# Kernel tuning notes

Measured on AMD Instinct MI355X. Metric: run time of the kernel, lower is better.

## Reference

```python
import jax, jax.numpy as jnp
import numpy as np

TOP_K = 2


def setup_inputs() -> dict:
    key = jax.random.key(0)
    ks = jax.random.split(key, 7)
    B, S, D, E = 8, 2048, 1024, 8
    scale = 1.0 / np.sqrt(D)
    return {
        "X": jax.random.normal(ks[0], (B, S, D), dtype=jnp.float32),
        "We": jax.random.normal(ks[1], (E, D, D), dtype=jnp.float32) * scale,
        "be": jax.random.normal(ks[2], (E, D), dtype=jnp.float32) * scale,
        "Wr": jax.random.normal(ks[3], (E, D), dtype=jnp.float32) * scale,
        "br": jax.random.normal(ks[4], (E,), dtype=jnp.float32) * scale,
        "Wo": jax.random.normal(ks[5], (D, D), dtype=jnp.float32) * scale,
        "bo": jax.random.normal(ks[6], (D,), dtype=jnp.float32) * scale,
    }


def reference(X, We, be, Wr, br, Wo, bo):
    # Router: logits [B, S, E] -> softmax -> top-k
    router_logits = jnp.einsum("bsd,ed->bse", X, Wr) + br
    router_weights = jax.nn.softmax(router_logits, axis=-1)
    top_k_weights, top_k_indices = jax.lax.top_k(router_weights, TOP_K)  # [B,S,K]

    # Every expert Linear applied to all tokens (matches original's dense-per-expert math).
    # expert_outputs: [B, S, E, D]
    expert_outputs = jnp.einsum("bsd,ehd->bseh", X, We) + be

    # Gather the top-k experts per token and combine with router weights.
    # gathered: [B, S, K, D]
    gathered = jnp.take_along_axis(expert_outputs, top_k_indices[..., None], axis=2)
    combined = jnp.sum(top_k_weights[..., None] * gathered, axis=2)  # [B, S, D]

    # Output projection
    out = jnp.einsum("bsd,hd->bsh", combined, Wo) + bo
    return out
```

## Files before the change

kernel.cpp:

```cpp
#include <hip/hip_runtime.h>
#include <stdint.h>

#define T_TOK 16384
#define D_DIM 1024
#define E_NUM 8
#define NTILE 264

typedef __attribute__((ext_vector_type(4))) float f32x4;
typedef __attribute__((ext_vector_type(8))) __bf16 bf16x8;
typedef __attribute__((ext_vector_type(4))) unsigned short u16x4;
typedef const __attribute__((address_space(1))) void* gas_ptr;
typedef __attribute__((address_space(3))) void* las_ptr;

#define WS_Y     0ULL
#define WS_ATOK  67108864ULL
#define WS_AW    (WS_ATOK + 131072ULL)
#define WS_SCHED (WS_AW + 131072ULL)
#define WS_TMP   (WS_SCHED + 8192ULL)
#define WS_TKI   WS_TMP
#define WS_TKW   (WS_TKI + 131072ULL)
#define WS_CNTS  (WS_TKW + 131072ULL)
#define WS_BASE  (WS_CNTS + 8192ULL)
#define WS_WOB   WS_TMP


__device__ __forceinline__ unsigned short f2b(float f){
  unsigned int u = __float_as_uint(f);
  u = (u + 0x7FFFu + ((u >> 16) & 1u)) >> 16;
  return (unsigned short)u;
}

__global__ __launch_bounds__(256) void k_router(const float* __restrict__ X,
    const float* __restrict__ Wr, const float* __restrict__ br,
    unsigned short* __restrict__ Xb, int* __restrict__ tki, float* __restrict__ tkw)
{
  const int wv = threadIdx.x >> 6, lane = threadIdx.x & 63;
  const int t = blockIdx.x * 4 + wv;
  const float* x = X + (size_t)t * D_DIM;
  unsigned short* xb = Xb + (size_t)t * D_DIM;
  float acc[E_NUM] = {};
  #pragma unroll
  for (int c = 0; c < 4; ++c){
    const int d = c * 256 + lane * 4;
    f32x4 xv = *reinterpret_cast<const f32x4*>(x + d);
    u16x4 o;
    o[0]=f2b(xv[0]); o[1]=f2b(xv[1]); o[2]=f2b(xv[2]); o[3]=f2b(xv[3]);
    *reinterpret_cast<u16x4*>(xb + d) = o;
    #pragma unroll
    for (int e = 0; e < E_NUM; ++e){
      f32x4 w4 = *reinterpret_cast<const f32x4*>(Wr + e * D_DIM + d);
      acc[e] += xv[0]*w4[0] + xv[1]*w4[1] + xv[2]*w4[2] + xv[3]*w4[3];
    }
  }
  #pragma unroll
  for (int e = 0; e < E_NUM; ++e){
    float v = acc[e];
    #pragma unroll
    for (int off = 32; off >= 1; off >>= 1) v += __shfl_xor(v, off, 64);
    acc[e] = v + br[e];
  }
  int i1 = 0; float l1 = acc[0];
  #pragma unroll
  for (int e = 1; e < E_NUM; ++e) if (acc[e] > l1){ l1 = acc[e]; i1 = e; }
  int i2 = -1; float l2 = -3.4e38f;
  #pragma unroll
  for (int e = 0; e < E_NUM; ++e) if (e != i1 && acc[e] > l2){ l2 = acc[e]; i2 = e; }
  float s = 0.f;
  #pragma unroll
  for (int e = 0; e < E_NUM; ++e) s += __expf(acc[e] - l1);
  if (lane == 0){
    tki[2*t] = i1; tki[2*t+1] = i2;
    tkw[2*t] = __expf(l1 - l1) / s; tkw[2*t+1] = __expf(l2 - l1) / s;
  }
}

__global__ void k_cvt(const float* __restrict__ in, unsigned short* __restrict__ out, int n4)
{
  int i = blockIdx.x * blockDim.x + threadIdx.x;
  if (i >= n4) return;
  f32x4 v = reinterpret_cast<const f32x4*>(in)[i];
  u16x4 o;
  o[0]=f2b(v[0]); o[1]=f2b(v[1]); o[2]=f2b(v[2]); o[3]=f2b(v[3]);
  reinterpret_cast<u16x4*>(out)[i] = o;
}

__global__ __launch_bounds__(64) void k_hist(const int* __restrict__ tki, int* __restrict__ cnts)
{
  const int b = blockIdx.x, lane = threadIdx.x;
  const int t = b * 64 + lane;
  const int e0 = tki[2*t], e1 = tki[2*t+1];
  #pragma unroll
  for (int ex = 0; ex < E_NUM; ++ex){
    unsigned long long m0 = __ballot(e0 == ex);
    unsigned long long m1 = __ballot(e1 == ex);
    if (lane == 0) cnts[b * E_NUM + ex] = __popcll(m0) + __popcll(m1);
  }
}

__global__ __launch_bounds__(64) void k_scan(const int* __restrict__ cnts,
    int* __restrict__ bases, int4* __restrict__ sched)
{
  const int lane = threadIdx.x;
  const int e = lane & 7, g = lane >> 3;
  int own = 0;
  for (int i = 0; i < 32; ++i) own += cnts[(g * 32 + i) * E_NUM + e];
  int incl = own;
  #pragma unroll
  for (int s = 8; s < 64; s <<= 1){
    int v = __shfl_up(incl, s, 64);
    if (lane >= s) incl += v;
  }
  int tot[E_NUM];
  #pragma unroll
  for (int ee = 0; ee < E_NUM; ++ee) tot[ee] = __shfl(incl, 56 + ee, 64);
  int offs_e = 0;
  #pragma unroll
  for (int ee = 0; ee < E_NUM; ++ee) if (ee < e) offs_e += tot[ee];
  int run = offs_e + (incl - own);
  for (int i = 0; i < 32; ++i){
    const int b = g * 32 + i;
    bases[b * E_NUM + e] = run;
    run += cnts[b * E_NUM + e];
  }
  if (lane == 0){
    int slot = 0, off = 0;
    for (int ee = 0; ee < E_NUM; ++ee){
      const int c = tot[ee];
      for (int tile = 0; tile * 128 < c && slot < NTILE; ++tile)
        sched[slot++] = make_int4(ee, off + tile * 128, min(128, c - tile * 128), 0);
      off += c;
    }
    while (slot < NTILE) sched[slot++] = make_int4(0, 0, 0, 0);
  }
}

__global__ __launch_bounds__(64) void k_scatter(const int* __restrict__ tki,
    const float* __restrict__ tkw, const int* __restrict__ bases,
    int* __restrict__ atok, float* __restrict__ aw)
{
  const int b = blockIdx.x, lane = threadIdx.x;
  const int t = b * 64 + lane;
  const unsigned long long lt = (1ull << lane) - 1ull;
  const int e0 = tki[2*t], e1 = tki[2*t+1];
  int r0 = 0, r1 = 0, p0c[E_NUM];
  #pragma unroll
  for (int ex = 0; ex < E_NUM; ++ex){
    unsigned long long m0 = __ballot(e0 == ex);
    p0c[ex] = __popcll(m0);
    if (e0 == ex) r0 = __popcll(m0 & lt);
  }
  #pragma unroll
  for (int ex = 0; ex < E_NUM; ++ex){
    unsigned long long m1 = __ballot(e1 == ex);
    if (e1 == ex) r1 = p0c[ex] + __popcll(m1 & lt);
  }
  const int row0 = bases[b * E_NUM + e0] + r0;
  const int row1 = bases[b * E_NUM + e1] + r1;
  atok[row0] = 2*t;     aw[row0] = tkw[2*t];
  atok[row1] = 2*t + 1; aw[row1] = tkw[2*t+1];
}

__global__ __launch_bounds__(256) void k_expert(const unsigned short* __restrict__ Xb,
    const unsigned short* __restrict__ Web, const float* __restrict__ be,
    const int4* __restrict__ sched, const int* __restrict__ atok,
    const float* __restrict__ aw, unsigned short* __restrict__ Y)
{
  __shared__ unsigned short As[128 * 64];
  __shared__ unsigned short Bs[128 * 64];
  __shared__ int   tok_s[128];
  __shared__ float w_s[128];

  const int lin = blockIdx.x;
  const int x = lin & 7, c = (lin >> 3) & 7, a = lin >> 6;
  const int j = x * 33 + a;
  const int4 sc = sched[j];
  const int e = sc.x, row0 = sc.y, nval = sc.z;
  const int n0 = c * 128;

  const int tid = threadIdx.x, wv = tid >> 6, lane = tid & 63;
  const int wm = wv >> 1, wn = wv & 1, lr = lane & 15, lg = lane >> 4;

  if (tid < 128){
    tok_s[tid] = atok[row0 + max(0, min(tid, nval - 1))];
    w_s[tid]   = aw[row0 + min(tid, 127)];
  }
  __syncthreads();

  const char* asrc[4]; const char* bsrc[4]; int ldso[4];
  #pragma unroll
  for (int i = 0; i < 4; ++i){
    const int chunk = i * 4 + wv;
    const int byte0 = chunk * 1024 + lane * 16;
    const int r = byte0 >> 7;
    const int cb = byte0 & 127;
    const int scb = cb ^ ((r & 7) << 4);
    asrc[i] = (const char*)(Xb + (size_t)(tok_s[r] >> 1) * D_DIM) + scb;
    bsrc[i] = (const char*)(Web + ((size_t)e * D_DIM + n0 + r) * D_DIM) + scb;
    ldso[i] = chunk * 512;
  }

  f32x4 acc[4][4] = {};
  #pragma unroll 1
  for (int kt = 0; kt < 16; ++kt){
    __syncthreads();
    #pragma unroll
    for (int i = 0; i < 4; ++i){
      __builtin_amdgcn_global_load_lds((gas_ptr)(asrc[i] + kt * 128), (las_ptr)(As + ldso[i]), 16, 0, 0);
      __builtin_amdgcn_global_load_lds((gas_ptr)(bsrc[i] + kt * 128), (las_ptr)(Bs + ldso[i]), 16, 0, 0);
    }
    __syncthreads();
    #pragma unroll
    for (int kk = 0; kk < 2; ++kk){
      bf16x8 af[4], bfr[4];
      #pragma unroll
      for (int fm = 0; fm < 4; ++fm){
        const int r = wm*64 + fm*16 + lr;
        af[fm] = *reinterpret_cast<const bf16x8*>((char*)As + ((r*128 + kk*64 + lg*16) ^ ((r & 7) << 4)));
      }
      #pragma unroll
      for (int fn = 0; fn < 4; ++fn){
        const int r = wn*64 + fn*16 + lr;
        bfr[fn] = *reinterpret_cast<const bf16x8*>((char*)Bs + ((r*128 + kk*64 + lg*16) ^ ((r & 7) << 4)));
      }
      #pragma unroll
      for (int fm = 0; fm < 4; ++fm)
        #pragma unroll
        for (int fn = 0; fn < 4; ++fn)
          acc[fm][fn] = __builtin_amdgcn_mfma_f32_16x16x32_bf16(af[fm], bfr[fn], acc[fm][fn], 0, 0, 0);
    }
  }

  float bev[4];
  #pragma unroll
  for (int fn = 0; fn < 4; ++fn) bev[fn] = be[e * D_DIM + n0 + wn*64 + fn*16 + lr];
  #pragma unroll
  for (int fm = 0; fm < 4; ++fm){
    #pragma unroll
    for (int jj = 0; jj < 4; ++jj){
      const int r = wm*64 + fm*16 + lg*4 + jj;
      if (r < nval){
        const float w = w_s[r];
        const size_t yrow = (size_t)tok_s[r];
        #pragma unroll
        for (int fn = 0; fn < 4; ++fn){
          const int col = n0 + wn*64 + fn*16 + lr;
          Y[yrow * D_DIM + col] = f2b(w * (acc[fm][fn][jj] + bev[fn]));
        }
      }
    }
  }
}

__global__ __launch_bounds__(256) void k_outproj(const unsigned short* __restrict__ Y,
    const unsigned short* __restrict__ Wob, const float* __restrict__ bo,
    float* __restrict__ out)
{
  __shared__ unsigned short As0[128 * 64];
  __shared__ unsigned short As1[128 * 64];
  __shared__ unsigned short Bs[128 * 64];

  const int lin = blockIdx.x;
  const int x = lin & 7, c = (lin >> 3) & 7, a = lin >> 6;
  const int tm = x * 16 + a;
  const int n0 = c * 128;

  const int tid = threadIdx.x, wv = tid >> 6, lane = tid & 63;
  const int wm = wv >> 1, wn = wv & 1, lr = lane & 15, lg = lane >> 4;

  const char* a0src[4]; const char* a1src[4]; const char* bsrc[4]; int ldso[4];
  #pragma unroll
  for (int i = 0; i < 4; ++i){
    const int chunk = i * 4 + wv;
    const int byte0 = chunk * 1024 + lane * 16;
    const int r = byte0 >> 7;
    const int cb = byte0 & 127;
    const int scb = cb ^ ((r & 7) << 4);
    const size_t t = (size_t)(tm * 128 + r);
    a0src[i] = (const char*)(Y + (2*t)     * D_DIM) + scb;
    a1src[i] = (const char*)(Y + (2*t + 1) * D_DIM) + scb;
    bsrc[i]  = (const char*)(Wob + (size_t)(n0 + r) * D_DIM) + scb;
    ldso[i] = chunk * 512;
  }

  f32x4 acc[4][4] = {};
  #pragma unroll 1
  for (int kt = 0; kt < 16; ++kt){
    __syncthreads();
    #pragma unroll
    for (int i = 0; i < 4; ++i){
      __builtin_amdgcn_global_load_lds((gas_ptr)(a0src[i] + kt * 128), (las_ptr)(As0 + ldso[i]), 16, 0, 0);
      __builtin_amdgcn_global_load_lds((gas_ptr)(a1src[i] + kt * 128), (las_ptr)(As1 + ldso[i]), 16, 0, 0);
      __builtin_amdgcn_global_load_lds((gas_ptr)(bsrc[i] + kt * 128), (las_ptr)(Bs  + ldso[i]), 16, 0, 0);
    }
    __syncthreads();
    #pragma unroll
    for (int kk = 0; kk < 2; ++kk){
      bf16x8 a0f[4], a1f[4], bfr[4];
      #pragma unroll
      for (int fm = 0; fm < 4; ++fm){
        const int r = wm*64 + fm*16 + lr;
        const int ba = (r*128 + kk*64 + lg*16) ^ ((r & 7) << 4);
        a0f[fm] = *reinterpret_cast<const bf16x8*>((char*)As0 + ba);
        a1f[fm] = *reinterpret_cast<const bf16x8*>((char*)As1 + ba);
      }
      #pragma unroll
      for (int fn = 0; fn < 4; ++fn){
        const int r = wn*64 + fn*16 + lr;
        bfr[fn] = *reinterpret_cast<const bf16x8*>((char*)Bs + ((r*128 + kk*64 + lg*16) ^ ((r & 7) << 4)));
      }
      #pragma unroll
      for (int fm = 0; fm < 4; ++fm)
        #pragma unroll
        for (int fn = 0; fn < 4; ++fn){
          acc[fm][fn] = __builtin_amdgcn_mfma_f32_16x16x32_bf16(a0f[fm], bfr[fn], acc[fm][fn], 0, 0, 0);
          acc[fm][fn] = __builtin_amdgcn_mfma_f32_16x16x32_bf16(a1f[fm], bfr[fn], acc[fm][fn], 0, 0, 0);
        }
    }
  }

  float bov[4];
  #pragma unroll
  for (int fn = 0; fn < 4; ++fn) bov[fn] = bo[n0 + wn*64 + fn*16 + lr];
  #pragma unroll
  for (int fm = 0; fm < 4; ++fm){
    #pragma unroll
    for (int jj = 0; jj < 4; ++jj){
      const int r = wm*64 + fm*16 + lg*4 + jj;
      #pragma unroll
      for (int fn = 0; fn < 4; ++fn){
        const int col = n0 + wn*64 + fn*16 + lr;
        out[(size_t)(tm * 128 + r) * D_DIM + col] = acc[fm][fn][jj] + bov[fn];
      }
    }
  }
}

extern "C" void kernel_launch(void* const* d_in, const int* in_sizes, int n_in,
                              void* d_out, int out_size, void* d_ws, size_t ws_size,
                              hipStream_t stream)
{
  const float* X  = (const float*)d_in[0];
  const float* We = (const float*)d_in[1];
  const float* be = (const float*)d_in[2];
  const float* Wr = (const float*)d_in[3];
  const float* br = (const float*)d_in[4];
  const float* Wo = (const float*)d_in[5];
  const float* bo = (const float*)d_in[6];
  float* out = (float*)d_out;
  char* ws = (char*)d_ws;

  unsigned short* Y   = (unsigned short*)(ws + WS_Y);
  int*   atok  = (int*)(ws + WS_ATOK);
  float* aw    = (float*)(ws + WS_AW);
  int4*  sched = (int4*)(ws + WS_SCHED);
  int*   tki   = (int*)(ws + WS_TKI);
  float* tkw   = (float*)(ws + WS_TKW);
  int*   cnts  = (int*)(ws + WS_CNTS);
  int*   bases = (int*)(ws + WS_BASE);
  unsigned short* Wob = (unsigned short*)(ws + WS_WOB);

  unsigned short* Xb  = (unsigned short*)d_out;
  unsigned short* Web = (unsigned short*)((char*)d_out + 33554432);

  k_router<<<T_TOK / 4, 256, 0, stream>>>(X, Wr, br, Xb, tki, tkw);
  k_cvt<<<(E_NUM * D_DIM * D_DIM / 4) / 256, 256, 0, stream>>>(We, Web, E_NUM * D_DIM * D_DIM / 4);
  k_hist<<<256, 64, 0, stream>>>(tki, cnts);
  k_scan<<<1, 64, 0, stream>>>(cnts, bases, sched);
  k_scatter<<<256, 64, 0, stream>>>(tki, tkw, bases, atok, aw);
  k_cvt<<<(D_DIM * D_DIM / 4) / 256, 256, 0, stream>>>(Wo, Wob, D_DIM * D_DIM / 4);
  k_expert<<<NTILE * 8, 256, 0, stream>>>(Xb, Web, be, sched, atok, aw, Y);
  k_outproj<<<1024, 256, 0, stream>>>(Y, Wob, bo, out);
}
```

Measured before the change: 352.5 us.

## Enlarge expert and output-projection GEMM M-tiles to 256 rows with 512-thread blocks

Expert and output-projection GEMMs move from 128x128 tiles with 256 threads to 256x128 tiles with 512 threads (8 waves), so each block reuses its B (weight) tile across twice as many rows. The schedule is rebuilt with 256-token tiles and NTILE is reduced to match, and the first top-k weight is simplified to 1/s. This is meant to cut redundant weight traffic and block count, at the cost of more LDS per block, possibly lower occupancy, and more padding waste on partially filled expert tiles.

```diff
diff --git a/kernel.cpp b/kernel.cpp
--- a/kernel.cpp
+++ b/kernel.cpp
@@ -4,7 +4,7 @@
 #define T_TOK 16384
 #define D_DIM 1024
 #define E_NUM 8
-#define NTILE 264
+#define NTILE 136
 
 typedef __attribute__((ext_vector_type(4))) float f32x4;
 typedef __attribute__((ext_vector_type(8))) __bf16 bf16x8;
@@ -70,7 +70,7 @@
   for (int e = 0; e < E_NUM; ++e) s += __expf(acc[e] - l1);
   if (lane == 0){
     tki[2*t] = i1; tki[2*t+1] = i2;
-    tkw[2*t] = __expf(l1 - l1) / s; tkw[2*t+1] = __expf(l2 - l1) / s;
+    tkw[2*t] = 1.0f / s; tkw[2*t+1] = __expf(l2 - l1) / s;
   }
 }
 
@@ -126,8 +126,8 @@
     int slot = 0, off = 0;
     for (int ee = 0; ee < E_NUM; ++ee){
       const int c = tot[ee];
-      for (int tile = 0; tile * 128 < c && slot < NTILE; ++tile)
-        sched[slot++] = make_int4(ee, off + tile * 128, min(128, c - tile * 128), 0);
+      for (int tile = 0; tile * 256 < c && slot < NTILE; ++tile)
+        sched[slot++] = make_int4(ee, off + tile * 256, min(256, c - tile * 256), 0);
       off += c;
     }
     while (slot < NTILE) sched[slot++] = make_int4(0, 0, 0, 0);
@@ -160,19 +160,19 @@
   atok[row1] = 2*t + 1; aw[row1] = tkw[2*t+1];
 }
 
-__global__ __launch_bounds__(256) void k_expert(const unsigned short* __restrict__ Xb,
+__global__ __launch_bounds__(512, 4) void k_expert(const unsigned short* __restrict__ Xb,
     const unsigned short* __restrict__ Web, const float* __restrict__ be,
     const int4* __restrict__ sched, const int* __restrict__ atok,
     const float* __restrict__ aw, unsigned short* __restrict__ Y)
 {
-  __shared__ unsigned short As[128 * 64];
+  __shared__ unsigned short As[256 * 64];
   __shared__ unsigned short Bs[128 * 64];
-  __shared__ int   tok_s[128];
-  __shared__ float w_s[128];
+  __shared__ int   tok_s[256];
+  __shared__ float w_s[256];
 
   const int lin = blockIdx.x;
   const int x = lin & 7, c = (lin >> 3) & 7, a = lin >> 6;
-  const int j = x * 33 + a;
+  const int j = x * 17 + a;
   const int4 sc = sched[j];
   const int e = sc.x, row0 = sc.y, nval = sc.z;
   const int n0 = c * 128;
@@ -180,23 +180,30 @@
   const int tid = threadIdx.x, wv = tid >> 6, lane = tid & 63;
   const int wm = wv >> 1, wn = wv & 1, lr = lane & 15, lg = lane >> 4;
 
-  if (tid < 128){
+  if (tid < 256){
     tok_s[tid] = atok[row0 + max(0, min(tid, nval - 1))];
-    w_s[tid]   = aw[row0 + min(tid, 127)];
+    w_s[tid]   = aw[row0 + min(tid, 255)];
   }
   __syncthreads();
 
-  const char* asrc[4]; const char* bsrc[4]; int ldso[4];
+  const char* asrc[4]; const char* bsrc[2]; int ldsoA[4], ldsoB[2];
   #pragma unroll
   for (int i = 0; i < 4; ++i){
-    const int chunk = i * 4 + wv;
+    const int chunk = i * 8 + wv;
     const int byte0 = chunk * 1024 + lane * 16;
     const int r = byte0 >> 7;
-    const int cb = byte0 & 127;
-    const int scb = cb ^ ((r & 7) << 4);
+    const int scb = (byte0 & 127) ^ ((r & 7) << 4);
     asrc[i] = (const char*)(Xb + (size_t)(tok_s[r] >> 1) * D_DIM) + scb;
+    ldsoA[i] = chunk * 512;
+  }
+  #pragma unroll
+  for (int i = 0; i < 2; ++i){
+    const int chunk = i * 8 + wv;
+    const int byte0 = chunk * 1024 + lane * 16;
+    const int r = byte0 >> 7;
+    const int scb = (byte0 & 127) ^ ((r & 7) << 4);
     bsrc[i] = (const char*)(Web + ((size_t)e * D_DIM + n0 + r) * D_DIM) + scb;
-    ldso[i] = chunk * 512;
+    ldsoB[i] = chunk * 512;
   }
 
   f32x4 acc[4][4] = {};
@@ -204,10 +211,11 @@
   for (int kt = 0; kt < 16; ++kt){
     __syncthreads();
     #pragma unroll
-    for (int i = 0; i < 4; ++i){
-      __builtin_amdgcn_global_load_lds((gas_ptr)(asrc[i] + kt * 128), (las_ptr)(As + ldso[i]), 16, 0, 0);
-      __builtin_amdgcn_global_load_lds((gas_ptr)(bsrc[i] + kt * 128), (las_ptr)(Bs + ldso[i]), 16, 0, 0);
-    }
+    for (int i = 0; i < 4; ++i)
+      __builtin_amdgcn_global_load_lds((gas_ptr)(asrc[i] + kt * 128), (las_ptr)(As + ldsoA[i]), 16, 0, 0);
+    #pragma unroll
+    for (int i = 0; i < 2; ++i)
+      __builtin_amdgcn_global_load_lds((gas_ptr)(bsrc[i] + kt * 128), (las_ptr)(Bs + ldsoB[i]), 16, 0, 0);
     __syncthreads();
     #pragma unroll
     for (int kk = 0; kk < 2; ++kk){
@@ -251,35 +259,42 @@
   }
 }
 
-__global__ __launch_bounds__(256) void k_outproj(const unsigned short* __restrict__ Y,
+__global__ __launch_bounds__(512, 4) void k_outproj(const unsigned short* __restrict__ Y,
     const unsigned short* __restrict__ Wob, const float* __restrict__ bo,
     float* __restrict__ out)
 {
-  __shared__ unsigned short As0[128 * 64];
-  __shared__ unsigned short As1[128 * 64];
+  __shared__ unsigned short As0[256 * 64];
+  __shared__ unsigned short As1[256 * 64];
   __shared__ unsigned short Bs[128 * 64];
 
   const int lin = blockIdx.x;
   const int x = lin & 7, c = (lin >> 3) & 7, a = lin >> 6;
-  const int tm = x * 16 + a;
+  const int tm = x * 8 + a;
   const int n0 = c * 128;
 
   const int tid = threadIdx.x, wv = tid >> 6, lane = tid & 63;
   const int wm = wv >> 1, wn = wv & 1, lr = lane & 15, lg = lane >> 4;
 
-  const char* a0src[4]; const char* a1src[4]; const char* bsrc[4]; int ldso[4];
+  const char* a0src[4]; const char* a1src[4]; const char* bsrc[2]; int ldsoA[4], ldsoB[2];
   #pragma unroll
   for (int i = 0; i < 4; ++i){
-    const int chunk = i * 4 + wv;
+    const int chunk = i * 8 + wv;
     const int byte0 = chunk * 1024 + lane * 16;
     const int r = byte0 >> 7;
-    const int cb = byte0 & 127;
-    const int scb = cb ^ ((r & 7) << 4);
-    const size_t t = (size_t)(tm * 128 + r);
+    const int scb = (byte0 & 127) ^ ((r & 7) << 4);
+    const size_t t = (size_t)(tm * 256 + r);
     a0src[i] = (const char*)(Y + (2*t)     * D_DIM) + scb;
     a1src[i] = (const char*)(Y + (2*t + 1) * D_DIM) + scb;
-    bsrc[i]  = (const char*)(Wob + (size_t)(n0 + r) * D_DIM) + scb;
-    ldso[i] = chunk * 512;
+    ldsoA[i] = chunk * 512;
+  }
+  #pragma unroll
+  for (int i = 0; i < 2; ++i){
+    const int chunk = i * 8 + wv;
+    const int byte0 = chunk * 1024 + lane * 16;
+    const int r = byte0 >> 7;
+    const int scb = (byte0 & 127) ^ ((r & 7) << 4);
+    bsrc[i] = (const char*)(Wob + (size_t)(n0 + r) * D_DIM) + scb;
+    ldsoB[i] = chunk * 512;
   }
 
   f32x4 acc[4][4] = {};
@@ -288,10 +303,12 @@
     __syncthreads();
     #pragma unroll
     for (int i = 0; i < 4; ++i){
-      __builtin_amdgcn_global_load_lds((gas_ptr)(a0src[i] + kt * 128), (las_ptr)(As0 + ldso[i]), 16, 0, 0);
-      __builtin_amdgcn_global_load_lds((gas_ptr)(a1src[i] + kt * 128), (las_ptr)(As1 + ldso[i]), 16, 0, 0);
-      __builtin_amdgcn_global_load_lds((gas_ptr)(bsrc[i] + kt * 128), (las_ptr)(Bs  + ldso[i]), 16, 0, 0);
-    }
+      __builtin_amdgcn_global_load_lds((gas_ptr)(a0src[i] + kt * 128), (las_ptr)(As0 + ldsoA[i]), 16, 0, 0);
+      __builtin_amdgcn_global_load_lds((gas_ptr)(a1src[i] + kt * 128), (las_ptr)(As1 + ldsoA[i]), 16, 0, 0);
+    }
+    #pragma unroll
+    for (int i = 0; i < 2; ++i)
+      __builtin_amdgcn_global_load_lds((gas_ptr)(bsrc[i] + kt * 128), (las_ptr)(Bs + ldsoB[i]), 16, 0, 0);
     __syncthreads();
     #pragma unroll
     for (int kk = 0; kk < 2; ++kk){
@@ -329,7 +346,7 @@
       #pragma unroll
       for (int fn = 0; fn < 4; ++fn){
         const int col = n0 + wn*64 + fn*16 + lr;
-        out[(size_t)(tm * 128 + r) * D_DIM + col] = acc[fm][fn][jj] + bov[fn];
+        out[(size_t)(tm * 256 + r) * D_DIM + col] = acc[fm][fn][jj] + bov[fn];
       }
     }
   }
@@ -368,6 +385,6 @@
   k_scan<<<1, 64, 0, stream>>>(cnts, bases, sched);
   k_scatter<<<256, 64, 0, stream>>>(tki, tkw, bases, atok, aw);
   k_cvt<<<(D_DIM * D_DIM / 4) / 256, 256, 0, stream>>>(Wo, Wob, D_DIM * D_DIM / 4);
-  k_expert<<<NTILE * 8, 256, 0, stream>>>(Xb, Web, be, sched, atok, aw, Y);
-  k_outproj<<<1024, 256, 0, stream>>>(Y, Wob, bo, out);
-}
+  k_expert<<<NTILE * 8, 512, 0, stream>>>(Xb, Web, be, sched, atok, aw, Y);
+  k_outproj<<<512, 512, 0, stream>>>(Y, Wob, bo, out);
+}
```

Measured after the change: 333.8 us. -5.3%, faster.
